# Kernel optimization log

Measured on AMD Instinct MI355X. Metric: run time of the kernel, lower is better.

Reference implementation:

```python
import jax, jax.numpy as jnp
import numpy as np

DIM_Z = 32      # latent Kalman state dim
DIM_Y = 16      # pseudo-observation dim
K_CLUST = 64    # number of switching clusters
T = 128         # sequence_length
BATCH = 256     # batch_size
INIT_COV = 20.0
NOISE_Q = 0.08  # noise_transition
NOISE_R = 0.03  # noise_emission
INIT_KF = 0.05  # init_kf_matrices (C init scale)


def setup_inputs() -> dict:
    key = jax.random.key(0)
    k1, k2, k3, k4, k5 = jax.random.split(key, 5)
    y = jax.random.normal(k1, (BATCH, T, DIM_Y), jnp.float32)
    dist = jax.random.normal(k2, (BATCH, T, K_CLUST), jnp.float32)
    # A initialized as identity per cluster (plus tiny perturbation so grads are non-trivial)
    A = jnp.broadcast_to(jnp.eye(DIM_Z, dtype=jnp.float32), (K_CLUST, DIM_Z, DIM_Z)) \
        + 0.01 * jax.random.normal(k3, (K_CLUST, DIM_Z, DIM_Z), jnp.float32)
    Bm = 0.01 * jax.random.normal(k4, (K_CLUST, DIM_Z), jnp.float32)  # bias (zeros-init in original)
    C = INIT_KF * jax.random.normal(k5, (K_CLUST, DIM_Y, DIM_Z), jnp.float32)
    return {"y": y, "dist": dist, "A": A, "Bm": Bm, "C": C}


def reference(y, dist, A, Bm, C):
    Q = NOISE_Q * jnp.eye(DIM_Z, dtype=y.dtype)
    R = NOISE_R * jnp.eye(DIM_Y, dtype=y.dtype)
    I = jnp.eye(DIM_Z, dtype=y.dtype)

    mu0 = jnp.zeros((BATCH, DIM_Z), y.dtype)
    Sigma0 = INIT_COV * jnp.broadcast_to(jnp.eye(DIM_Z, dtype=y.dtype), (BATCH, DIM_Z, DIM_Z))
    # first time instant: alpha from dist at t=0 (alphaDistProb ~ softmax over clusters)
    alpha0 = jax.nn.softmax(dist[:, 0, :], axis=-1)

    ys_t = jnp.swapaxes(y, 0, 1)      # [T, B, dim_y]
    dist_t = jnp.swapaxes(dist, 0, 1)  # [T, B, K]

    def step(carry, xs):
        mu_pred, Sigma_pred, alpha = carry
        yt, dt = xs
        # --- update: alpha-mixed emission matrix ---
        C_t = jnp.einsum('bk,kyz->byz', alpha, C)                     # [B, y, z]
        innov = yt - jnp.einsum('byz,bz->by', C_t, mu_pred)
        S = jnp.einsum('byz,bzw,bxw->byx', C_t, Sigma_pred, C_t) + R  # [B, y, y]
        S_inv = jnp.linalg.inv(S)
        K_g = jnp.einsum('bzw,byw,byx->bzx', Sigma_pred, C_t, S_inv)  # Kalman gain [B, z, y]
        mu_f = mu_pred + jnp.einsum('bzy,by->bz', K_g, innov)
        I_KC = I - jnp.einsum('bzy,byw->bzw', K_g, C_t)
        Sigma_f = jnp.einsum('bij,bjk->bik', I_KC, Sigma_pred)
        # --- alpha update (update_alpha_CG_KVAE: combine cluster evidence with prev alpha) ---
        p = jax.nn.softmax(dt, axis=-1) * alpha
        alpha_new = p / jnp.sum(p, axis=-1, keepdims=True)
        # --- predict: alpha-mixed transition ---
        A_t = jnp.einsum('bk,kij->bij', alpha_new, A)
        B_t = alpha_new @ Bm
        mu_pred_new = jnp.einsum('bij,bj->bi', A_t, mu_f) + B_t
        Sigma_pred_new = jnp.einsum('bij,bjk,blk->bil', A_t, Sigma_f, A_t) + Q
        outs = (mu_pred, Sigma_pred, mu_f, Sigma_f, alpha_new, A_t, B_t, C_t)
        return (mu_pred_new, Sigma_pred_new, alpha_new), outs

    _, stacked = jax.lax.scan(step, (mu0, Sigma0, alpha0), (ys_t, dist_t))
    # (mu_preds, Sigma_preds, mu_filts, Sigma_filts, alphas, As, Bs, Cs), each time-major [T, B, ...]
    return stacked
```

## Files before the change

kernel.cpp:

```cpp
#include <hip/hip_runtime.h>

#define TT 128
#define BB 256
#define KC 64
#define DZ 32
#define DY 16

#define OFF_MUP   ((size_t)0)
#define OFF_SIGP  (OFF_MUP  + (size_t)TT*BB*DZ)
#define OFF_MUF   (OFF_SIGP + (size_t)TT*BB*DZ*DZ)
#define OFF_SIGF  (OFF_MUF  + (size_t)TT*BB*DZ)
#define OFF_ALPHA (OFF_SIGF + (size_t)TT*BB*DZ*DZ)
#define OFF_AS    (OFF_ALPHA+ (size_t)TT*BB*KC)
#define OFF_BS    (OFF_AS   + (size_t)TT*BB*DZ*DZ)
#define OFF_CS    (OFF_BS   + (size_t)TT*BB*DZ)

__device__ __forceinline__ float wave_max64(float v) {
#pragma unroll
  for (int o = 32; o > 0; o >>= 1) v = fmaxf(v, __shfl_xor(v, o, 64));
  return v;
}
__device__ __forceinline__ float wave_sum64(float v) {
#pragma unroll
  for (int o = 32; o > 0; o >>= 1) v += __shfl_xor(v, o, 64);
  return v;
}

__global__ __launch_bounds__(64) void alpha_kernel(const float* __restrict__ dist,
                                                   float* __restrict__ alphas,
                                                   float* __restrict__ beta0) {
  const int b = blockIdx.x;
  const int k = threadIdx.x;
  const float* db = dist + (size_t)b * TT * KC;

  float d0 = db[k];
  float m0 = wave_max64(d0);
  float e0 = expf(d0 - m0);
  float s0 = wave_sum64(e0);
  float carry = e0 / s0;
  beta0[b * KC + k] = carry;

  for (int t = 0; t < TT; ++t) {
    float d = db[t * KC + k];
    float mm = wave_max64(d);
    float ee = expf(d - mm);
    float ss = wave_sum64(ee);
    float p = (ee / ss) * carry;
    float ps = wave_sum64(p);
    float a = p / ps;
    alphas[((size_t)t * BB + b) * KC + k] = a;
    carry = a;
  }
}

__global__ __launch_bounds__(256) void mix_kernel(const float* __restrict__ A,
                                                  const float* __restrict__ Bm,
                                                  const float* __restrict__ C,
                                                  const float* __restrict__ alphas,
                                                  const float* __restrict__ beta0,
                                                  float* __restrict__ As,
                                                  float* __restrict__ Bs,
                                                  float* __restrict__ Cs) {
  const int g   = blockIdx.x;
  const int t   = g >> 3;
  const int b0  = (g & 7) << 5;
  const int tid = threadIdx.x;
  const float* arow = alphas + ((size_t)t * BB + b0) * KC;
  const float* brow = (t > 0) ? (alphas + ((size_t)(t - 1) * BB + b0) * KC)
                              : (beta0 + (size_t)b0 * KC);
  const size_t rbase = (size_t)t * BB + b0;

  {
    const float4* wp = (const float4*)A;
    for (int ch = 0; ch < 2; ++ch) {
      float4 acc[16];
#pragma unroll
      for (int r = 0; r < 16; ++r) acc[r] = make_float4(0.f, 0.f, 0.f, 0.f);
      for (int kk = 0; kk < KC; ++kk) {
        float4 w = wp[kk * 256 + tid];
#pragma unroll
        for (int r = 0; r < 16; ++r) {
          float a = arow[(ch * 16 + r) * KC + kk];
          acc[r].x += a * w.x; acc[r].y += a * w.y;
          acc[r].z += a * w.z; acc[r].w += a * w.w;
        }
      }
#pragma unroll
      for (int r = 0; r < 16; ++r)
        ((float4*)(As + (rbase + ch * 16 + r) * (DZ * DZ)))[tid] = acc[r];
    }
  }
  if (tid < 128) {
    const float4* wp = (const float4*)C;
    for (int ch = 0; ch < 2; ++ch) {
      float4 acc[16];
#pragma unroll
      for (int r = 0; r < 16; ++r) acc[r] = make_float4(0.f, 0.f, 0.f, 0.f);
      for (int kk = 0; kk < KC; ++kk) {
        float4 w = wp[kk * 128 + tid];
#pragma unroll
        for (int r = 0; r < 16; ++r) {
          float a = brow[(ch * 16 + r) * KC + kk];
          acc[r].x += a * w.x; acc[r].y += a * w.y;
          acc[r].z += a * w.z; acc[r].w += a * w.w;
        }
      }
#pragma unroll
      for (int r = 0; r < 16; ++r)
        ((float4*)(Cs + (rbase + ch * 16 + r) * (DY * DZ)))[tid] = acc[r];
    }
  } else if (tid < 192) {
    const int c = (tid - 128) & 7;
    const float4* wp = (const float4*)Bm;
    for (int ch = 0; ch < 2; ++ch) {
      float4 acc[16];
#pragma unroll
      for (int r = 0; r < 16; ++r) acc[r] = make_float4(0.f, 0.f, 0.f, 0.f);
      for (int kk = 0; kk < KC; ++kk) {
        float4 w = wp[kk * 8 + c];
#pragma unroll
        for (int r = 0; r < 16; ++r) {
          float a = arow[(ch * 16 + r) * KC + kk];
          acc[r].x += a * w.x; acc[r].y += a * w.y;
          acc[r].z += a * w.z; acc[r].w += a * w.w;
        }
      }
#pragma unroll
      for (int r = 0; r < 16; ++r)
        ((float4*)(Bs + (rbase + ch * 16 + r) * DZ))[c] = acc[r];
    }
  }
}

__global__ __launch_bounds__(256) void kf_kernel(const float* __restrict__ yin,
                                                 const float* __restrict__ As,
                                                 const float* __restrict__ Bs,
                                                 const float* __restrict__ Cs,
                                                 float* __restrict__ out) {
  const int b   = blockIdx.x;
  const int tid = threadIdx.x;

  __shared__ float Sig[DZ][36];
  __shared__ float Sf [DZ][36];
  __shared__ float Mm [DZ][36];
  __shared__ float At [DZ][36];
  __shared__ float AtT[DZ][36];
  __shared__ float CtT[DZ][24];
  __shared__ float PCt[DZ][24];
  __shared__ float PCtT[DY][36];
  __shared__ float KgT[DY][36];
  __shared__ float W[DY][52];
  __shared__ float mu[DZ], muf[DZ], innov[DY], Bt[DZ], ytl[DY];

  const int i  = tid >> 3;
  const int j0 = (tid & 7) * 4;

  {
#pragma unroll
    for (int q = 0; q < 4; ++q) Sig[i][j0 + q] = (i == j0 + q) ? 20.0f : 0.0f;
    if (tid < DZ) mu[tid] = 0.0f;
  }
  __syncthreads();

  for (int t = 0; t < TT; ++t) {
    const size_t tb = (size_t)t * BB + b;

    {
      float4 a4 = *(const float4*)(As + tb * (DZ * DZ) + i * DZ + j0);
      *(float4*)&At[i][j0] = a4;
      AtT[j0 + 0][i] = a4.x; AtT[j0 + 1][i] = a4.y;
      AtT[j0 + 2][i] = a4.z; AtT[j0 + 3][i] = a4.w;
      if (tid < 128) {
        int yy = tid >> 3;
        float4 c4 = *(const float4*)(Cs + tb * (DY * DZ) + yy * DZ + j0);
        CtT[j0 + 0][yy] = c4.x; CtT[j0 + 1][yy] = c4.y;
        CtT[j0 + 2][yy] = c4.z; CtT[j0 + 3][yy] = c4.w;
      } else if (tid < 160) {
        Bt[tid - 128] = Bs[tb * DZ + (tid - 128)];
      } else if (tid < 176) {
        ytl[tid - 160] = yin[((size_t)b * TT + t) * DY + (tid - 160)];
      }
      float4 s4 = *(float4*)&Sig[i][j0];
      *(float4*)(out + OFF_SIGP + tb * (DZ * DZ) + i * DZ + j0) = s4;
      if (tid < DZ) out[OFF_MUP + tb * DZ + tid] = mu[tid];
    }
    __syncthreads();

    if (tid < 128) {
      int z = tid >> 2, x0 = (tid & 3) * 4;
      float4 acc = make_float4(0.f, 0.f, 0.f, 0.f);
      for (int w = 0; w < DZ; ++w) {
        float s = Sig[z][w];
        float4 c = *(float4*)&CtT[w][x0];
        acc.x += s * c.x; acc.y += s * c.y; acc.z += s * c.z; acc.w += s * c.w;
      }
      *(float4*)&PCt[z][x0] = acc;
      PCtT[x0 + 0][z] = acc.x; PCtT[x0 + 1][z] = acc.y;
      PCtT[x0 + 2][z] = acc.z; PCtT[x0 + 3][z] = acc.w;
      W[x0 + 0][16 + z] = acc.x; W[x0 + 1][16 + z] = acc.y;
      W[x0 + 2][16 + z] = acc.z; W[x0 + 3][16 + z] = acc.w;
    } else if (tid < 144) {
      int yy = tid - 128;
      float a = ytl[yy];
      for (int z = 0; z < DZ; ++z) a -= CtT[z][yy] * mu[z];
      innov[yy] = a;
    }
    __syncthreads();

    if (tid < 64) {
      int yy = tid >> 2, x0 = (tid & 3) * 4;
      float4 acc = make_float4(0.f, 0.f, 0.f, 0.f);
      for (int z = 0; z < DZ; ++z) {
        float cv = CtT[z][yy];
        float4 pv = *(float4*)&PCt[z][x0];
        acc.x += cv * pv.x; acc.y += cv * pv.y; acc.z += cv * pv.z; acc.w += cv * pv.w;
      }
      if (yy >= x0 && yy < x0 + 4) (&acc.x)[yy - x0] += 0.03f;
      *(float4*)&W[yy][x0] = acc;
    }
    __syncthreads();

    if (tid < 64) {
      const int q  = tid >> 2;
      const int cg = tid & 3;
      for (int p = 0; p < 16; ++p) {
        float pinv = 1.0f / W[p][p];
        if (q != p) {
          float mql = W[q][p] * pinv;
#pragma unroll
          for (int rr = 0; rr < 3; ++rr) {
            int c = (cg + rr * 4) * 4;
            float4 pv = *(float4*)&W[p][c];
            float4 qv = *(float4*)&W[q][c];
            qv.x -= mql * pv.x; qv.y -= mql * pv.y;
            qv.z -= mql * pv.z; qv.w -= mql * pv.w;
            *(float4*)&W[q][c] = qv;
          }
        }
      }
#pragma unroll
      for (int rep = 0; rep < 2; ++rep) {
        int job = tid + rep * 64;
        int yy = job >> 3, z0 = (job & 7) * 4;
        float dinv = 1.0f / W[yy][yy];
        float4 v = *(float4*)&W[yy][16 + z0];
        v.x *= dinv; v.y *= dinv; v.z *= dinv; v.w *= dinv;
        *(float4*)&KgT[yy][z0] = v;
      }
    }
    __syncthreads();

    {
      float4 acc = *(float4*)&Sig[i][j0];
      for (int yy = 0; yy < DY; ++yy) {
        float kg = KgT[yy][i];
        float4 pv = *(float4*)&PCtT[yy][j0];
        acc.x -= kg * pv.x; acc.y -= kg * pv.y; acc.z -= kg * pv.z; acc.w -= kg * pv.w;
      }
      *(float4*)&Sf[i][j0] = acc;
      *(float4*)(out + OFF_SIGF + tb * (DZ * DZ) + i * DZ + j0) = acc;
      if (tid < DZ) {
        float a = mu[tid];
        for (int yy = 0; yy < DY; ++yy) a += KgT[yy][tid] * innov[yy];
        muf[tid] = a;
      }
    }
    __syncthreads();

    {
      float4 acc = make_float4(0.f, 0.f, 0.f, 0.f);
      for (int k = 0; k < DZ; ++k) {
        float av = At[i][k];
        float4 sv = *(float4*)&Sf[k][j0];
        acc.x += av * sv.x; acc.y += av * sv.y; acc.z += av * sv.z; acc.w += av * sv.w;
      }
      *(float4*)&Mm[i][j0] = acc;
      if (tid < DZ) out[OFF_MUF + tb * DZ + tid] = muf[tid];
    }
    __syncthreads();

    {
      float4 acc = make_float4(0.f, 0.f, 0.f, 0.f);
      for (int k = 0; k < DZ; ++k) {
        float mv = Mm[i][k];
        float4 av = *(float4*)&AtT[k][j0];
        acc.x += mv * av.x; acc.y += mv * av.y; acc.z += mv * av.z; acc.w += mv * av.w;
      }
      if (i >= j0 && i < j0 + 4) (&acc.x)[i - j0] += 0.08f;
      *(float4*)&Sig[i][j0] = acc;
      if (tid < DZ) {
        float a = Bt[tid];
        for (int k = 0; k < DZ; ++k) a += At[tid][k] * muf[k];
        mu[tid] = a;
      }
    }
    __syncthreads();
  }
}

extern "C" void kernel_launch(void* const* d_in, const int* in_sizes, int n_in,
                              void* d_out, int out_size, void* d_ws, size_t ws_size,
                              hipStream_t stream) {
  const float* y    = (const float*)d_in[0];
  const float* dist = (const float*)d_in[1];
  const float* A    = (const float*)d_in[2];
  const float* Bm   = (const float*)d_in[3];
  const float* C    = (const float*)d_in[4];
  float* out   = (float*)d_out;
  float* beta0 = (float*)d_ws;

  hipLaunchKernelGGL(alpha_kernel, dim3(BB), dim3(64), 0, stream,
                     dist, out + OFF_ALPHA, beta0);
  hipLaunchKernelGGL(mix_kernel, dim3(TT * BB / 32), dim3(256), 0, stream,
                     A, Bm, C, out + OFF_ALPHA, beta0,
                     out + OFF_AS, out + OFF_BS, out + OFF_CS);
  hipLaunchKernelGGL(kf_kernel, dim3(BB), dim3(256), 0, stream,
                     y, out + OFF_AS, out + OFF_BS, out + OFF_CS, out);
}
```

Before: 1.495 ms.

## Parallelize alpha recursion in log space and restructure Kalman step kernel

The alpha recursion is reformulated as a prefix sum of log-softmax terms, so four waves each handle a chunk of the time axis instead of one wave walking sequentially. The mixing kernel stages the alpha rows in shared memory. The Kalman kernel prefetches the next step's A, B, C and y into registers, fuses the S build, Gauss-Jordan inversion and innovation into one stage using register shuffles, splits reductions across more threads, and replaces __syncthreads with a lighter barrier macro. The log-space reformulation can change numerics when probabilities underflow, and the custom barrier depends on LDS-only waitcnt semantics being sufficient.

```diff
diff --git a/kernel.cpp b/kernel.cpp
--- a/kernel.cpp
+++ b/kernel.cpp
@@ -1,4 +1,5 @@
 #include <hip/hip_runtime.h>
+#include <math.h>
 
 #define TT 128
 #define BB 256
@@ -15,6 +16,10 @@
 #define OFF_BS    (OFF_AS   + (size_t)TT*BB*DZ*DZ)
 #define OFF_CS    (OFF_BS   + (size_t)TT*BB*DZ)
 
+#define BAR() do { asm volatile("s_waitcnt lgkmcnt(0)" ::: "memory"); \
+                   __builtin_amdgcn_s_barrier(); \
+                   asm volatile("" ::: "memory"); } while (0)
+
 __device__ __forceinline__ float wave_max64(float v) {
 #pragma unroll
   for (int o = 32; o > 0; o >>= 1) v = fmaxf(v, __shfl_xor(v, o, 64));
@@ -25,31 +30,53 @@
   for (int o = 32; o > 0; o >>= 1) v += __shfl_xor(v, o, 64);
   return v;
 }
-
-__global__ __launch_bounds__(64) void alpha_kernel(const float* __restrict__ dist,
-                                                   float* __restrict__ alphas,
-                                                   float* __restrict__ beta0) {
+__device__ __forceinline__ float4 shfl4(const float4& v, int src) {
+  return make_float4(__shfl(v.x, src, 64), __shfl(v.y, src, 64),
+                     __shfl(v.z, src, 64), __shfl(v.w, src, 64));
+}
+__device__ __forceinline__ float f4get(const float4& v, int e) {
+  return e == 0 ? v.x : (e == 1 ? v.y : (e == 2 ? v.z : v.w));
+}
+
+__global__ __launch_bounds__(256) void alpha_kernel(const float* __restrict__ dist,
+                                                    float* __restrict__ alphas,
+                                                    float* __restrict__ beta0) {
   const int b = blockIdx.x;
-  const int k = threadIdx.x;
+  const int w = threadIdx.x >> 6;
+  const int lane = threadIdx.x & 63;
   const float* db = dist + (size_t)b * TT * KC;
 
-  float d0 = db[k];
-  float m0 = wave_max64(d0);
-  float e0 = expf(d0 - m0);
-  float s0 = wave_sum64(e0);
-  float carry = e0 / s0;
-  beta0[b * KC + k] = carry;
-
-  for (int t = 0; t < TT; ++t) {
-    float d = db[t * KC + k];
-    float mm = wave_max64(d);
-    float ee = expf(d - mm);
-    float ss = wave_sum64(ee);
-    float p = (ee / ss) * carry;
-    float ps = wave_sum64(p);
-    float a = p / ps;
-    alphas[((size_t)t * BB + b) * KC + k] = a;
-    carry = a;
+  __shared__ float ls[TT][KC];
+  __shared__ float chT[4][KC];
+  __shared__ float l0[KC];
+
+  float csum = 0.f;
+  for (int tt = 0; tt < 32; ++tt) {
+    int t = w * 32 + tt;
+    float d = db[t * KC + lane];
+    float m = wave_max64(d);
+    float e = expf(d - m);
+    float s = wave_sum64(e);
+    float lsv = d - m - logf(s);
+    ls[t][lane] = lsv;
+    csum += lsv;
+    if (t == 0) l0[lane] = lsv;
+  }
+  chT[w][lane] = csum;
+  __syncthreads();
+
+  float off = l0[lane];
+  for (int w2 = 0; w2 < w; ++w2) off += chT[w2][lane];
+  if (threadIdx.x < 64) beta0[b * KC + lane] = expf(l0[lane]);
+
+  float run = off;
+  for (int tt = 0; tt < 32; ++tt) {
+    int t = w * 32 + tt;
+    run += ls[t][lane];
+    float m = wave_max64(run);
+    float e = expf(run - m);
+    float s = wave_sum64(e);
+    alphas[((size_t)t * BB + b) * KC + lane] = e / s;
   }
 }
 
@@ -70,6 +97,14 @@
                               : (beta0 + (size_t)b0 * KC);
   const size_t rbase = (size_t)t * BB + b0;
 
+  __shared__ float aS[32][KC];
+  __shared__ float bS[32][KC];
+  ((float4*)aS)[tid]       = ((const float4*)arow)[tid];
+  ((float4*)aS)[tid + 256] = ((const float4*)arow)[tid + 256];
+  ((float4*)bS)[tid]       = ((const float4*)brow)[tid];
+  ((float4*)bS)[tid + 256] = ((const float4*)brow)[tid + 256];
+  __syncthreads();
+
   {
     const float4* wp = (const float4*)A;
     for (int ch = 0; ch < 2; ++ch) {
@@ -77,12 +112,12 @@
 #pragma unroll
       for (int r = 0; r < 16; ++r) acc[r] = make_float4(0.f, 0.f, 0.f, 0.f);
       for (int kk = 0; kk < KC; ++kk) {
-        float4 w = wp[kk * 256 + tid];
+        float4 wv = wp[kk * 256 + tid];
 #pragma unroll
         for (int r = 0; r < 16; ++r) {
-          float a = arow[(ch * 16 + r) * KC + kk];
-          acc[r].x += a * w.x; acc[r].y += a * w.y;
-          acc[r].z += a * w.z; acc[r].w += a * w.w;
+          float a = aS[ch * 16 + r][kk];
+          acc[r].x += a * wv.x; acc[r].y += a * wv.y;
+          acc[r].z += a * wv.z; acc[r].w += a * wv.w;
         }
       }
 #pragma unroll
@@ -97,12 +132,12 @@
 #pragma unroll
       for (int r = 0; r < 16; ++r) acc[r] = make_float4(0.f, 0.f, 0.f, 0.f);
       for (int kk = 0; kk < KC; ++kk) {
-        float4 w = wp[kk * 128 + tid];
+        float4 wv = wp[kk * 128 + tid];
 #pragma unroll
         for (int r = 0; r < 16; ++r) {
-          float a = brow[(ch * 16 + r) * KC + kk];
-          acc[r].x += a * w.x; acc[r].y += a * w.y;
-          acc[r].z += a * w.z; acc[r].w += a * w.w;
+          float a = bS[ch * 16 + r][kk];
+          acc[r].x += a * wv.x; acc[r].y += a * wv.y;
+          acc[r].z += a * wv.z; acc[r].w += a * wv.w;
         }
       }
 #pragma unroll
@@ -117,12 +152,12 @@
 #pragma unroll
       for (int r = 0; r < 16; ++r) acc[r] = make_float4(0.f, 0.f, 0.f, 0.f);
       for (int kk = 0; kk < KC; ++kk) {
-        float4 w = wp[kk * 8 + c];
+        float4 wv = wp[kk * 8 + c];
 #pragma unroll
         for (int r = 0; r < 16; ++r) {
-          float a = arow[(ch * 16 + r) * KC + kk];
-          acc[r].x += a * w.x; acc[r].y += a * w.y;
-          acc[r].z += a * w.z; acc[r].w += a * w.w;
+          float a = aS[ch * 16 + r][kk];
+          acc[r].x += a * wv.x; acc[r].y += a * wv.y;
+          acc[r].z += a * wv.z; acc[r].w += a * wv.w;
         }
       }
 #pragma unroll
@@ -149,126 +184,143 @@
   __shared__ float PCt[DZ][24];
   __shared__ float PCtT[DY][36];
   __shared__ float KgT[DY][36];
-  __shared__ float W[DY][52];
-  __shared__ float mu[DZ], muf[DZ], innov[DY], Bt[DZ], ytl[DY];
+  __shared__ __align__(16) float mu[DZ];
+  __shared__ __align__(16) float muf[DZ];
+  __shared__ __align__(16) float Bt[DZ];
+  __shared__ float innov[DY], ytl[DY];
 
   const int i  = tid >> 3;
   const int j0 = (tid & 7) * 4;
 
+#pragma unroll
+  for (int q = 0; q < 4; ++q) Sig[i][j0 + q] = (i == j0 + q) ? 20.0f : 0.0f;
+  if (tid < DZ) mu[tid] = 0.0f;
+
+  float4 pA, pC = make_float4(0.f, 0.f, 0.f, 0.f);
+  float  pB = 0.f, pY = 0.f;
   {
-#pragma unroll
-    for (int q = 0; q < 4; ++q) Sig[i][j0 + q] = (i == j0 + q) ? 20.0f : 0.0f;
-    if (tid < DZ) mu[tid] = 0.0f;
-  }
-  __syncthreads();
+    const size_t tb0 = (size_t)b;
+    pA = *(const float4*)(As + tb0 * (DZ * DZ) + tid * 4);
+    if (tid < 128)      pC = *(const float4*)(Cs + tb0 * (DY * DZ) + tid * 4);
+    else if (tid < 160) pB = Bs[tb0 * DZ + (tid - 128)];
+    else if (tid < 176) pY = yin[(size_t)b * TT * DY + (tid - 160)];
+  }
 
   for (int t = 0; t < TT; ++t) {
     const size_t tb = (size_t)t * BB + b;
 
-    {
-      float4 a4 = *(const float4*)(As + tb * (DZ * DZ) + i * DZ + j0);
-      *(float4*)&At[i][j0] = a4;
-      AtT[j0 + 0][i] = a4.x; AtT[j0 + 1][i] = a4.y;
-      AtT[j0 + 2][i] = a4.z; AtT[j0 + 3][i] = a4.w;
-      if (tid < 128) {
-        int yy = tid >> 3;
-        float4 c4 = *(const float4*)(Cs + tb * (DY * DZ) + yy * DZ + j0);
-        CtT[j0 + 0][yy] = c4.x; CtT[j0 + 1][yy] = c4.y;
-        CtT[j0 + 2][yy] = c4.z; CtT[j0 + 3][yy] = c4.w;
-      } else if (tid < 160) {
-        Bt[tid - 128] = Bs[tb * DZ + (tid - 128)];
-      } else if (tid < 176) {
-        ytl[tid - 160] = yin[((size_t)b * TT + t) * DY + (tid - 160)];
-      }
+    *(float4*)&At[i][j0] = pA;
+    AtT[j0 + 0][i] = pA.x; AtT[j0 + 1][i] = pA.y;
+    AtT[j0 + 2][i] = pA.z; AtT[j0 + 3][i] = pA.w;
+    if (tid < 128) {
+      int yy = tid >> 3;
+      CtT[j0 + 0][yy] = pC.x; CtT[j0 + 1][yy] = pC.y;
+      CtT[j0 + 2][yy] = pC.z; CtT[j0 + 3][yy] = pC.w;
+    } else if (tid < 160) Bt[tid - 128] = pB;
+    else if (tid < 176)   ytl[tid - 160] = pY;
+
+    {
       float4 s4 = *(float4*)&Sig[i][j0];
-      *(float4*)(out + OFF_SIGP + tb * (DZ * DZ) + i * DZ + j0) = s4;
+      *(float4*)(out + OFF_SIGP + tb * (DZ * DZ) + tid * 4) = s4;
       if (tid < DZ) out[OFF_MUP + tb * DZ + tid] = mu[tid];
     }
-    __syncthreads();
-
-    if (tid < 128) {
-      int z = tid >> 2, x0 = (tid & 3) * 4;
+    {
+      int tn = (t + 1 < TT) ? (t + 1) : t;
+      size_t tbn = (size_t)tn * BB + b;
+      pA = *(const float4*)(As + tbn * (DZ * DZ) + tid * 4);
+      if (tid < 128)      pC = *(const float4*)(Cs + tbn * (DY * DZ) + tid * 4);
+      else if (tid < 160) pB = Bs[tbn * DZ + (tid - 128)];
+      else if (tid < 176) pY = yin[((size_t)b * TT + tn) * DY + (tid - 160)];
+    }
+    BAR();
+
+    {
+      const int z = tid >> 3, xg = (tid >> 1) & 3, h = tid & 1;
+      const int x0 = xg * 4, kb = h * 16;
       float4 acc = make_float4(0.f, 0.f, 0.f, 0.f);
-      for (int w = 0; w < DZ; ++w) {
-        float s = Sig[z][w];
-        float4 c = *(float4*)&CtT[w][x0];
+#pragma unroll
+      for (int k2 = 0; k2 < 16; ++k2) {
+        float s = Sig[z][kb + k2];
+        float4 c = *(float4*)&CtT[kb + k2][x0];
         acc.x += s * c.x; acc.y += s * c.y; acc.z += s * c.z; acc.w += s * c.w;
       }
-      *(float4*)&PCt[z][x0] = acc;
-      PCtT[x0 + 0][z] = acc.x; PCtT[x0 + 1][z] = acc.y;
-      PCtT[x0 + 2][z] = acc.z; PCtT[x0 + 3][z] = acc.w;
-      W[x0 + 0][16 + z] = acc.x; W[x0 + 1][16 + z] = acc.y;
-      W[x0 + 2][16 + z] = acc.z; W[x0 + 3][16 + z] = acc.w;
-    } else if (tid < 144) {
-      int yy = tid - 128;
-      float a = ytl[yy];
-      for (int z = 0; z < DZ; ++z) a -= CtT[z][yy] * mu[z];
-      innov[yy] = a;
-    }
-    __syncthreads();
+      acc.x += __shfl_xor(acc.x, 1, 64); acc.y += __shfl_xor(acc.y, 1, 64);
+      acc.z += __shfl_xor(acc.z, 1, 64); acc.w += __shfl_xor(acc.w, 1, 64);
+      if (h == 0) {
+        *(float4*)&PCt[z][x0] = acc;
+        PCtT[x0 + 0][z] = acc.x; PCtT[x0 + 1][z] = acc.y;
+        PCtT[x0 + 2][z] = acc.z; PCtT[x0 + 3][z] = acc.w;
+      }
+    }
+    BAR();
 
     if (tid < 64) {
-      int yy = tid >> 2, x0 = (tid & 3) * 4;
-      float4 acc = make_float4(0.f, 0.f, 0.f, 0.f);
+      const int q = tid >> 2, cg = tid & 3, x0 = cg * 4, base = tid & ~3;
+      float4 w0 = make_float4(0.f, 0.f, 0.f, 0.f);
+#pragma unroll 8
       for (int z = 0; z < DZ; ++z) {
-        float cv = CtT[z][yy];
+        float cv = CtT[z][q];
         float4 pv = *(float4*)&PCt[z][x0];
-        acc.x += cv * pv.x; acc.y += cv * pv.y; acc.z += cv * pv.z; acc.w += cv * pv.w;
-      }
-      if (yy >= x0 && yy < x0 + 4) (&acc.x)[yy - x0] += 0.03f;
-      *(float4*)&W[yy][x0] = acc;
-    }
-    __syncthreads();
-
-    if (tid < 64) {
-      const int q  = tid >> 2;
-      const int cg = tid & 3;
+        w0.x += cv * pv.x; w0.y += cv * pv.y; w0.z += cv * pv.z; w0.w += cv * pv.w;
+      }
+      w0.x += (q == x0 + 0) ? 0.03f : 0.f;
+      w0.y += (q == x0 + 1) ? 0.03f : 0.f;
+      w0.z += (q == x0 + 2) ? 0.03f : 0.f;
+      w0.w += (q == x0 + 3) ? 0.03f : 0.f;
+      float4 w1 = *(float4*)&PCtT[q][x0];
+      float4 w2 = *(float4*)&PCtT[q][x0 + 16];
+#pragma unroll
       for (int p = 0; p < 16; ++p) {
-        float pinv = 1.0f / W[p][p];
-        if (q != p) {
-          float mql = W[q][p] * pinv;
-#pragma unroll
-          for (int rr = 0; rr < 3; ++rr) {
-            int c = (cg + rr * 4) * 4;
-            float4 pv = *(float4*)&W[p][c];
-            float4 qv = *(float4*)&W[q][c];
-            qv.x -= mql * pv.x; qv.y -= mql * pv.y;
-            qv.z -= mql * pv.z; qv.w -= mql * pv.w;
-            *(float4*)&W[q][c] = qv;
-          }
-        }
-      }
-#pragma unroll
-      for (int rep = 0; rep < 2; ++rep) {
-        int job = tid + rep * 64;
-        int yy = job >> 3, z0 = (job & 7) * 4;
-        float dinv = 1.0f / W[yy][yy];
-        float4 v = *(float4*)&W[yy][16 + z0];
-        v.x *= dinv; v.y *= dinv; v.z *= dinv; v.w *= dinv;
-        *(float4*)&KgT[yy][z0] = v;
-      }
-    }
-    __syncthreads();
+        float4 pr0 = shfl4(w0, 4 * p + cg);
+        float4 pr1 = shfl4(w1, 4 * p + cg);
+        float4 pr2 = shfl4(w2, 4 * p + cg);
+        float pp  = __shfl(f4get(w0, p & 3), 4 * p + (p >> 2), 64);
+        float wqp = __shfl(f4get(w0, p & 3), base + (p >> 2), 64);
+        float m = (q == p) ? 0.f : (wqp * (1.0f / pp));
+        w0.x -= m * pr0.x; w0.y -= m * pr0.y; w0.z -= m * pr0.z; w0.w -= m * pr0.w;
+        w1.x -= m * pr1.x; w1.y -= m * pr1.y; w1.z -= m * pr1.z; w1.w -= m * pr1.w;
+        w2.x -= m * pr2.x; w2.y -= m * pr2.y; w2.z -= m * pr2.z; w2.w -= m * pr2.w;
+      }
+      float4 dblk = shfl4(w0, base + (q >> 2));
+      float dq = f4get(dblk, q & 3);
+      float di = 1.0f / dq;
+      *(float4*)&KgT[q][x0]      = make_float4(w1.x * di, w1.y * di, w1.z * di, w1.w * di);
+      *(float4*)&KgT[q][x0 + 16] = make_float4(w2.x * di, w2.y * di, w2.z * di, w2.w * di);
+    } else if (tid < 128) {
+      const int l = tid - 64, yy = l >> 2, zc = (l & 3) * 8;
+      float a = 0.f;
+#pragma unroll
+      for (int r = 0; r < 8; ++r) a += CtT[zc + r][yy] * mu[zc + r];
+      a += __shfl_xor(a, 1, 64);
+      a += __shfl_xor(a, 2, 64);
+      if ((l & 3) == 0) innov[yy] = ytl[yy] - a;
+    }
+    BAR();
 
     {
       float4 acc = *(float4*)&Sig[i][j0];
+#pragma unroll
       for (int yy = 0; yy < DY; ++yy) {
         float kg = KgT[yy][i];
         float4 pv = *(float4*)&PCtT[yy][j0];
         acc.x -= kg * pv.x; acc.y -= kg * pv.y; acc.z -= kg * pv.z; acc.w -= kg * pv.w;
       }
       *(float4*)&Sf[i][j0] = acc;
-      *(float4*)(out + OFF_SIGF + tb * (DZ * DZ) + i * DZ + j0) = acc;
-      if (tid < DZ) {
-        float a = mu[tid];
-        for (int yy = 0; yy < DY; ++yy) a += KgT[yy][tid] * innov[yy];
-        muf[tid] = a;
-      }
-    }
-    __syncthreads();
+      *(float4*)(out + OFF_SIGF + tb * (DZ * DZ) + tid * 4) = acc;
+      if (j0 < 16) {
+        float s = 0.f;
+#pragma unroll
+        for (int r = 0; r < 4; ++r) s += KgT[j0 + r][i] * innov[j0 + r];
+        s += __shfl_xor(s, 1, 64);
+        s += __shfl_xor(s, 2, 64);
+        if ((tid & 3) == 0) muf[i] = mu[i] + s;
+      }
+    }
+    BAR();
 
     {
       float4 acc = make_float4(0.f, 0.f, 0.f, 0.f);
+#pragma unroll 8
       for (int k = 0; k < DZ; ++k) {
         float av = At[i][k];
         float4 sv = *(float4*)&Sf[k][j0];
@@ -277,24 +329,31 @@
       *(float4*)&Mm[i][j0] = acc;
       if (tid < DZ) out[OFF_MUF + tb * DZ + tid] = muf[tid];
     }
-    __syncthreads();
+    BAR();
 
     {
       float4 acc = make_float4(0.f, 0.f, 0.f, 0.f);
+#pragma unroll 8
       for (int k = 0; k < DZ; ++k) {
         float mv = Mm[i][k];
         float4 av = *(float4*)&AtT[k][j0];
         acc.x += mv * av.x; acc.y += mv * av.y; acc.z += mv * av.z; acc.w += mv * av.w;
       }
-      if (i >= j0 && i < j0 + 4) (&acc.x)[i - j0] += 0.08f;
+      acc.x += (i == j0 + 0) ? 0.08f : 0.f;
+      acc.y += (i == j0 + 1) ? 0.08f : 0.f;
+      acc.z += (i == j0 + 2) ? 0.08f : 0.f;
+      acc.w += (i == j0 + 3) ? 0.08f : 0.f;
       *(float4*)&Sig[i][j0] = acc;
-      if (tid < DZ) {
-        float a = Bt[tid];
-        for (int k = 0; k < DZ; ++k) a += At[tid][k] * muf[k];
-        mu[tid] = a;
-      }
-    }
-    __syncthreads();
+
+      float4 a4 = *(float4*)&At[i][j0];
+      float4 m4 = *(float4*)&muf[j0];
+      float s = a4.x * m4.x + a4.y * m4.y + a4.z * m4.z + a4.w * m4.w;
+      s += __shfl_xor(s, 1, 64);
+      s += __shfl_xor(s, 2, 64);
+      s += __shfl_xor(s, 4, 64);
+      if ((tid & 7) == 0) mu[i] = Bt[i] + s;
+    }
+    BAR();
   }
 }
 
@@ -309,7 +368,7 @@
   float* out   = (float*)d_out;
   float* beta0 = (float*)d_ws;
 
-  hipLaunchKernelGGL(alpha_kernel, dim3(BB), dim3(64), 0, stream,
+  hipLaunchKernelGGL(alpha_kernel, dim3(BB), dim3(256), 0, stream,
                      dist, out + OFF_ALPHA, beta0);
   hipLaunchKernelGGL(mix_kernel, dim3(TT * BB / 32), dim3(256), 0, stream,
                      A, Bm, C, out + OFF_ALPHA, beta0,
```

After: 1.295 ms. -13.4%, faster.
